# Kernel tuning notes

Measured on AMD Instinct MI355X. Metric: run time of the kernel, lower is better.

## Reference

```python
import jax, jax.numpy as jnp
import numpy as np

K = 3          # kernel size
SH, SW = 2, 1  # stride
PH, PW = 1, 1  # padding


def conv2d(x, w, b, stride, pad):
    y = jax.lax.conv_general_dilated(
        x, w, window_strides=stride,
        padding=[(pad[0], pad[0]), (pad[1], pad[1])],
        dimension_numbers=('NCHW', 'OIHW', 'NCHW'))
    return y + b[None, :, None, None]


def setup_inputs() -> dict:
    key = jax.random.key(0)
    ks = jax.random.split(key, 4)
    x = jax.random.normal(ks[0], (8, 64, 128, 128), jnp.float32)
    # scale offset weights small so sampled offsets are O(1) pixels (exercises
    # the bilinear path without sampling far out of bounds)
    w_offset = jax.random.normal(ks[1], (18, 64, 3, 3), jnp.float32) * 0.02
    b_offset = jnp.zeros((18,), jnp.float32)
    w_mask = jax.random.normal(ks[2], (9, 64, 3, 3), jnp.float32) * 0.05
    b_mask = jnp.zeros((9,), jnp.float32)
    w_conv = jax.random.normal(ks[3], (64, 64, 3, 3), jnp.float32) * (1.0 / 24.0)
    return dict(x=x, w_offset=w_offset, b_offset=b_offset,
                w_mask=w_mask, b_mask=b_mask, w_conv=w_conv)


def _bilinear_gather(x, py, px):
    # x: [B,C,H,W]; py, px: [B,K2,Ho,Wo] float sampling coordinates.
    # Zero-padding outside the image (torchvision deform_conv2d semantics).
    B, C, H, W = x.shape
    y0f = jnp.floor(py)
    x0f = jnp.floor(px)
    dy = py - y0f
    dx = px - x0f
    y0 = y0f.astype(jnp.int32)
    x0 = x0f.astype(jnp.int32)

    def corner(yi, xi, wgt):
        valid = (yi >= 0) & (yi < H) & (xi >= 0) & (xi < W)
        yc = jnp.clip(yi, 0, H - 1)
        xc = jnp.clip(xi, 0, W - 1)
        # per-batch fancy gather -> [B, C, K2, Ho, Wo]
        g = jax.vmap(lambda xb, yb, xbi: xb[:, yb, xbi])(x, yc, xc)
        return g * (wgt * valid)[:, None]

    return (corner(y0,     x0,     (1 - dy) * (1 - dx))
            + corner(y0,     x0 + 1, (1 - dy) * dx)
            + corner(y0 + 1, x0,     dy * (1 - dx))
            + corner(y0 + 1, x0 + 1, dy * dx))


def reference(x, w_offset, b_offset, w_mask, b_mask, w_conv):
    B, C, H, W = x.shape
    offset = conv2d(x, w_offset, b_offset, (SH, SW), (PH, PW))   # [B, 2*K2, Ho, Wo]
    mask = jax.nn.sigmoid(conv2d(x, w_mask, b_mask, (SH, SW), (PH, PW)))  # [B, K2, Ho, Wo]
    Ho, Wo = offset.shape[2], offset.shape[3]
    K2 = K * K
    off = offset.reshape(B, K2, 2, Ho, Wo)
    off_y = off[:, :, 0]   # [B,K2,Ho,Wo]
    off_x = off[:, :, 1]
    ky = (jnp.arange(K2) // K).astype(jnp.float32)
    kx = (jnp.arange(K2) % K).astype(jnp.float32)
    hs = (jnp.arange(Ho) * SH - PH).astype(jnp.float32)
    ws = (jnp.arange(Wo) * SW - PW).astype(jnp.float32)
    py = off_y + ky[None, :, None, None] + hs[None, None, :, None]
    px = off_x + kx[None, :, None, None] + ws[None, None, None, :]
    sampled = _bilinear_gather(x, py, px) * mask[:, None]  # [B,C,K2,Ho,Wo]
    # weighted accumulate over in-channels and kernel taps
    out = jnp.einsum('ock,bckhw->bohw', w_conv.reshape(-1, C, K2), sampled)
    return out
```

## Files before the change

### kernel.cpp

```cpp
#include <hip/hip_runtime.h>
#include <hip/hip_bf16.h>
#include <math.h>

#define BB 8
#define CC 64
#define HH 128
#define WW 128
#define HO 64
#define WO 128
#define OC 64
#define HW (HH * WW)
#define HOWO (HO * WO)

typedef __attribute__((ext_vector_type(8))) short short8;
typedef __attribute__((ext_vector_type(4))) float floatx4;

union BfBits { __hip_bfloat16 h; unsigned short s; };
__device__ __forceinline__ unsigned short f2bf(float f) {
    BfBits b; b.h = __float2bfloat16(f); return b.s;
}
__device__ __forceinline__ float bflo(unsigned int u) {
    return __uint_as_float(u << 16);
}
__device__ __forceinline__ float bfhi(unsigned int u) {
    return __uint_as_float(u & 0xFFFF0000u);
}

__global__ __launch_bounds__(512) void prep(
    const float* __restrict__ x,
    const float* __restrict__ w_off, const float* __restrict__ w_msk,
    const float* __restrict__ w_conv,
    unsigned short* __restrict__ xT, unsigned int* __restrict__ xP,
    unsigned short* __restrict__ Wom, unsigned short* __restrict__ W2)
{
    __shared__ float T[64][129];
    int tid = threadIdx.x;
    int bx = blockIdx.x;
    if (bx < 1024) {
        int b = bx & 7, y = bx >> 3;
        int wl = tid & 127, c0 = tid >> 7;
#pragma unroll
        for (int i = 0; i < 16; ++i) {
            int c = 4 * i + c0;
            T[c][wl] = x[(((size_t)b * CC + c) * HH + y) * WW + wl];
        }
        __syncthreads();
        int c = tid & 63, wg = tid >> 6;
#pragma unroll
        for (int i = 0; i < 16; ++i) {
            int wp = wg * 16 + i;
            unsigned int lo = f2bf(T[c][wp]);
            unsigned int hi = (wp < 127) ? f2bf(T[c][wp + 1]) : 0u;
            size_t e = (((size_t)b * HH + y) * WW + wp) * 64 + c;
            xT[e] = (unsigned short)lo;
            xP[e] = lo | (hi << 16);
        }
    } else if (bx < 1060) {
        int i = (bx - 1024) * 512 + tid;
        int ch = i / 576, kk = i % 576;
        int xs = kk >> 6, c = kk & 63;
        float v = 0.0f;
        if (ch < 18)      v = w_off[(ch * CC + c) * 9 + xs];
        else if (ch < 27) v = w_msk[((ch - 18) * CC + c) * 9 + xs];
        Wom[i] = f2bf(v);
    } else {
        int i = (bx - 1060) * 512 + tid;
        int k = i % 9, c = (i / 9) % CC, o = i / (CC * 9);
        W2[((size_t)k * OC + o) * CC + c] = f2bf(w_conv[i]);
    }
}

__global__ __launch_bounds__(256) void fused(
    const unsigned short* __restrict__ xT, const unsigned int* __restrict__ xP,
    const unsigned short* __restrict__ Wom, const unsigned short* __restrict__ W2,
    const float* __restrict__ b_off, const float* __restrict__ b_msk,
    float* __restrict__ out)
{
    __shared__ __align__(16) char lds[47360];
    unsigned short (*S)[32][64] = (unsigned short(*)[32][64])lds;
    typedef unsigned short XsRow[34][72];
    XsRow* Xs = (XsRow*)lds;
    float (*omr)[33] = (float(*)[33])(lds + 36864);
    uint2*  metaR = (uint2*)(lds + 40432);
    float4* metaC = (float4*)(lds + 42736);

    int tid = threadIdx.x;
    int lane = tid & 63;
    int wv = __builtin_amdgcn_readfirstlane(tid >> 6);
    int bx = blockIdx.x;
    int b = bx & 7;
    int rest = bx >> 3;
    int h = rest >> 2;
    int w0 = (rest & 3) * 32;
    int h2 = 2 * h - 1;
    int m16 = lane & 15, q = lane >> 4;

    for (int u = tid; u < 816; u += 256) {
        int ky = u / 272;
        int rem = u - ky * 272;
        int col = rem >> 3, cb = rem & 7;
        int hy = h2 + ky, wc = w0 - 1 + col;
        short8 v = {0, 0, 0, 0, 0, 0, 0, 0};
        if ((unsigned)hy < (unsigned)HH && (unsigned)wc < (unsigned)WW)
            v = *(const short8*)(xT + (((size_t)b * HH + hy) * WW + wc) * 64 + cb * 8);
        *(short8*)&Xs[ky][col][cb * 8] = v;
    }
    __syncthreads();

    {
        int mt = wv & 1, nt = wv >> 1;
        floatx4 a = (floatx4){0.f, 0.f, 0.f, 0.f};
        const unsigned short* wa = Wom + (mt * 16 + m16) * 576 + q * 8;
#pragma unroll
        for (int t = 0; t < 18; ++t) {
            int xs = t >> 1, ky = xs / 3, kx = xs % 3;
            short8 af = *(const short8*)(wa + t * 32);
            short8 bf = *(const short8*)&Xs[ky][nt * 16 + m16 + kx][(t & 1) * 32 + q * 8];
            a = __builtin_amdgcn_mfma_f32_16x16x32_bf16(af, bf, a, 0, 0, 0);
        }
#pragma unroll
        for (int r = 0; r < 4; ++r) {
            int ch = mt * 16 + q * 4 + r;
            if (ch < 27) omr[ch][nt * 16 + m16] = a[r];
        }
    }
    __syncthreads();

    for (int u = tid; u < 288; u += 256) {
        int kk = u >> 5, pos = u & 31;
        float offy = omr[2 * kk][pos] + b_off[2 * kk];
        float offx = omr[2 * kk + 1][pos] + b_off[2 * kk + 1];
        float mk = 1.0f / (1.0f + __expf(-(omr[18 + kk][pos] + b_msk[kk])));
        float py = offy + (float)(kk / 3) + (float)h2;
        float px = offx + (float)(kk % 3) + (float)(w0 + pos - 1);

        float y0f = floorf(py), x0f = floorf(px);
        float dy = py - y0f, dx = px - x0f;
        int y0 = (int)y0f, x0 = (int)x0f;
        int y1 = y0 + 1, x1 = x0 + 1;
        bool vy0 = (unsigned)y0 < (unsigned)HH;
        bool vy1 = (unsigned)y1 < (unsigned)HH;
        bool vx0 = (unsigned)x0 < (unsigned)WW;
        bool vx1 = (unsigned)x1 < (unsigned)WW;
        float w00 = (1.0f - dy) * (1.0f - dx) * ((vy0 && vx0) ? mk : 0.0f);
        float w01 = (1.0f - dy) * dx          * ((vy0 && vx1) ? mk : 0.0f);
        float w10 = dy * (1.0f - dx)          * ((vy1 && vx0) ? mk : 0.0f);
        float w11 = dy * dx                   * ((vy1 && vx1) ? mk : 0.0f);
        int xbase = min(max(x0, 0), WW - 2);
        bool s0 = x0 > xbase;
        bool s1 = x1 > xbase;
        float4 cf;
        cf.x = (s0 ? 0.f : w00) + (s1 ? 0.f : w01);
        cf.y = (s0 ? w00 : 0.f) + (s1 ? w01 : 0.f);
        cf.z = (s0 ? 0.f : w10) + (s1 ? 0.f : w11);
        cf.w = (s0 ? w10 : 0.f) + (s1 ? w11 : 0.f);
        int yc0 = min(max(y0, 0), HH - 1);
        int yc1 = min(max(y1, 0), HH - 1);
        metaC[u] = cf;
        uint2 mr;
        mr.x = (unsigned)(yc0 * WW + xbase) * 256u;
        mr.y = (unsigned)(yc1 * WW + xbase) * 256u;
        metaR[u] = mr;
    }
    __syncthreads();

    int p0 = wv * 8;
    int c = lane;
    int c4 = 4 * c;
    const char* xPb = (const char*)(xP + (size_t)b * HW * 64);
    unsigned int G0[2][8], G1[2][8];

    auto issue = [&](int k, int sel) {
#pragma unroll
        for (int i = 0; i < 8; ++i) {
            uint2 mr = metaR[k * 32 + p0 + i];
            unsigned r0 = __builtin_amdgcn_readfirstlane(mr.x);
            unsigned r1 = __builtin_amdgcn_readfirstlane(mr.y);
            G0[sel][i] = *(const unsigned int*)(xPb + r0 + c4);
            G1[sel][i] = *(const unsigned int*)(xPb + r1 + c4);
        }
    };
    auto store = [&](int k, int sel) {
#pragma unroll
        for (int i = 0; i < 8; ++i) {
            float4 cf = metaC[k * 32 + p0 + i];
            float v = cf.x * bflo(G0[sel][i]) + cf.y * bfhi(G0[sel][i])
                    + cf.z * bflo(G1[sel][i]) + cf.w * bfhi(G1[sel][i]);
            int pos = p0 + i;
            S[k][pos][((c >> 3) ^ (pos & 7)) * 8 + (c & 7)] = f2bf(v);
        }
    };

    issue(0, 0);
#pragma unroll
    for (int k = 0; k < 9; ++k) {
        if (k < 8) issue(k + 1, (k + 1) & 1);
        store(k, k & 1);
    }
    __syncthreads();

    floatx4 acc0 = (floatx4){0.f, 0.f, 0.f, 0.f};
    floatx4 acc1 = (floatx4){0.f, 0.f, 0.f, 0.f};
#pragma unroll
    for (int k = 0; k < 9; ++k) {
        const unsigned short* wk = W2 + ((size_t)(k * OC) + wv * 16 + m16) * CC + q * 8;
#pragma unroll
        for (int s = 0; s < 2; ++s) {
            short8 af = *(const short8*)(wk + s * 32);
            int cb = ((q + 4 * s) ^ (m16 & 7)) * 8;
            short8 bf0 = *(const short8*)&S[k][m16][cb];
            short8 bf1 = *(const short8*)&S[k][16 + m16][cb];
            acc0 = __builtin_amdgcn_mfma_f32_16x16x32_bf16(af, bf0, acc0, 0, 0, 0);
            acc1 = __builtin_amdgcn_mfma_f32_16x16x32_bf16(af, bf1, acc1, 0, 0, 0);
        }
    }

#pragma unroll
    for (int nt = 0; nt < 2; ++nt) {
        floatx4 av = nt ? acc1 : acc0;
#pragma unroll
        for (int r = 0; r < 4; ++r) {
            int o = wv * 16 + q * 4 + r;
            out[(((size_t)b * OC + o) * HO + h) * WO + w0 + nt * 16 + m16] = av[r];
        }
    }
}

extern "C" void kernel_launch(void* const* d_in, const int* in_sizes, int n_in,
                              void* d_out, int out_size, void* d_ws, size_t ws_size,
                              hipStream_t stream)
{
    const float* x      = (const float*)d_in[0];
    const float* w_off  = (const float*)d_in[1];
    const float* b_off  = (const float*)d_in[2];
    const float* w_msk  = (const float*)d_in[3];
    const float* b_msk  = (const float*)d_in[4];
    const float* w_conv = (const float*)d_in[5];
    float* out = (float*)d_out;

    unsigned short* xT = (unsigned short*)d_ws;
    unsigned int* xP = (unsigned int*)(xT + (size_t)BB * HW * 64);
    unsigned short* Wom = (unsigned short*)(xP + (size_t)BB * HW * 64);
    unsigned short* W2 = Wom + 32 * 576;

    prep<<<dim3(1132), dim3(512), 0, stream>>>(x, w_off, w_msk, w_conv,
                                               xT, xP, Wom, W2);
    fused<<<dim3(2048), dim3(256), 0, stream>>>(xT, xP, Wom, W2,
                                                b_off, b_msk, out);
}
```

Before: 145.5 us.

## Pack 2x2 bilinear quads per pixel and pipeline gather with MFMA in halved LDS

Result: slower. 173.1 us (+18.9%).

```diff
diff --git a/kernel.cpp b/kernel.cpp
--- a/kernel.cpp
+++ b/kernel.cpp
@@ -1,5 +1,6 @@
 #include <hip/hip_runtime.h>
 #include <hip/hip_bf16.h>
+#include <hip/hip_fp16.h>
 #include <math.h>
 
 #define BB 8
@@ -30,30 +31,37 @@
     const float* __restrict__ x,
     const float* __restrict__ w_off, const float* __restrict__ w_msk,
     const float* __restrict__ w_conv,
-    unsigned short* __restrict__ xT, unsigned int* __restrict__ xP,
+    unsigned short* __restrict__ xT, uint2* __restrict__ xQ,
     unsigned short* __restrict__ Wom, unsigned short* __restrict__ W2)
 {
-    __shared__ float T[64][129];
+    __shared__ float T0[64][129];
+    __shared__ float T1[64][129];
     int tid = threadIdx.x;
     int bx = blockIdx.x;
     if (bx < 1024) {
         int b = bx & 7, y = bx >> 3;
         int wl = tid & 127, c0 = tid >> 7;
+        bool has1 = (y < 127);
 #pragma unroll
         for (int i = 0; i < 16; ++i) {
             int c = 4 * i + c0;
-            T[c][wl] = x[(((size_t)b * CC + c) * HH + y) * WW + wl];
+            const float* px = x + (((size_t)b * CC + c) * HH + y) * WW + wl;
+            T0[c][wl] = px[0];
+            T1[c][wl] = has1 ? px[WW] : 0.0f;
         }
         __syncthreads();
         int c = tid & 63, wg = tid >> 6;
 #pragma unroll
         for (int i = 0; i < 16; ++i) {
             int wp = wg * 16 + i;
-            unsigned int lo = f2bf(T[c][wp]);
-            unsigned int hi = (wp < 127) ? f2bf(T[c][wp + 1]) : 0u;
+            unsigned int lo0 = f2bf(T0[c][wp]);
+            unsigned int hi0 = (wp < 127) ? f2bf(T0[c][wp + 1]) : 0u;
+            unsigned int lo1 = f2bf(T1[c][wp]);
+            unsigned int hi1 = (wp < 127) ? f2bf(T1[c][wp + 1]) : 0u;
             size_t e = (((size_t)b * HH + y) * WW + wp) * 64 + c;
-            xT[e] = (unsigned short)lo;
-            xP[e] = lo | (hi << 16);
+            xT[e] = (unsigned short)lo0;
+            uint2 qv; qv.x = lo0 | (hi0 << 16); qv.y = lo1 | (hi1 << 16);
+            xQ[e] = qv;
         }
     } else if (bx < 1060) {
         int i = (bx - 1024) * 512 + tid;
@@ -71,18 +79,18 @@
 }
 
 __global__ __launch_bounds__(256) void fused(
-    const unsigned short* __restrict__ xT, const unsigned int* __restrict__ xP,
+    const unsigned short* __restrict__ xT, const uint2* __restrict__ xQ,
     const unsigned short* __restrict__ Wom, const unsigned short* __restrict__ W2,
     const float* __restrict__ b_off, const float* __restrict__ b_msk,
     float* __restrict__ out)
 {
-    __shared__ __align__(16) char lds[47360];
-    unsigned short (*S)[32][64] = (unsigned short(*)[32][64])lds;
+    __shared__ __align__(16) char lds[18304];
     typedef unsigned short XsRow[34][72];
     XsRow* Xs = (XsRow*)lds;
-    float (*omr)[33] = (float(*)[33])(lds + 36864);
-    uint2*  metaR = (uint2*)(lds + 40432);
-    float4* metaC = (float4*)(lds + 42736);
+    unsigned short (*S)[32][64] = (unsigned short(*)[32][64])lds;
+    unsigned int* metaR = (unsigned int*)(lds + 8192);
+    uint2* metaC = (uint2*)(lds + 9344);
+    float (*omr)[33] = (float(*)[33])(lds + 14720);
 
     int tid = threadIdx.x;
     int lane = tid & 63;
@@ -146,73 +154,82 @@
         float w01 = (1.0f - dy) * dx          * ((vy0 && vx1) ? mk : 0.0f);
         float w10 = dy * (1.0f - dx)          * ((vy1 && vx0) ? mk : 0.0f);
         float w11 = dy * dx                   * ((vy1 && vx1) ? mk : 0.0f);
-        int xbase = min(max(x0, 0), WW - 2);
-        bool s0 = x0 > xbase;
-        bool s1 = x1 > xbase;
-        float4 cf;
-        cf.x = (s0 ? 0.f : w00) + (s1 ? 0.f : w01);
-        cf.y = (s0 ? w00 : 0.f) + (s1 ? w01 : 0.f);
-        cf.z = (s0 ? 0.f : w10) + (s1 ? 0.f : w11);
-        cf.w = (s0 ? w10 : 0.f) + (s1 ? w11 : 0.f);
-        int yc0 = min(max(y0, 0), HH - 1);
-        int yc1 = min(max(y1, 0), HH - 1);
-        metaC[u] = cf;
-        uint2 mr;
-        mr.x = (unsigned)(yc0 * WW + xbase) * 256u;
-        mr.y = (unsigned)(yc1 * WW + xbase) * 256u;
-        metaR[u] = mr;
+        int yb = min(max(y0, 0), HH - 2);
+        int xb = min(max(x0, 0), WW - 2);
+        int a0 = min(max(y0 - yb, 0), 1);
+        int a1 = min(max(y1 - yb, 0), 1);
+        int e0 = min(max(x0 - xb, 0), 1);
+        int e1 = min(max(x1 - xb, 0), 1);
+        float r0A = ((e0 == 0) ? w00 : 0.f) + ((e1 == 0) ? w01 : 0.f);
+        float r0B = ((e0 == 1) ? w00 : 0.f) + ((e1 == 1) ? w01 : 0.f);
+        float r1A = ((e0 == 0) ? w10 : 0.f) + ((e1 == 0) ? w11 : 0.f);
+        float r1B = ((e0 == 1) ? w10 : 0.f) + ((e1 == 1) ? w11 : 0.f);
+        float c00 = ((a0 == 0) ? r0A : 0.f) + ((a1 == 0) ? r1A : 0.f);
+        float c01 = ((a0 == 0) ? r0B : 0.f) + ((a1 == 0) ? r1B : 0.f);
+        float c10 = ((a0 == 1) ? r0A : 0.f) + ((a1 == 1) ? r1A : 0.f);
+        float c11 = ((a0 == 1) ? r0B : 0.f) + ((a1 == 1) ? r1B : 0.f);
+
+        __half2 hA = __floats2half2_rn(c00, c01);
+        __half2 hB = __floats2half2_rn(c10, c11);
+        uint2 cc;
+        cc.x = __builtin_bit_cast(unsigned int, hA);
+        cc.y = __builtin_bit_cast(unsigned int, hB);
+        metaC[u] = cc;
+        metaR[u] = (unsigned)(yb * WW + xb) * 512u;
     }
     __syncthreads();
 
     int p0 = wv * 8;
     int c = lane;
-    int c4 = 4 * c;
-    const char* xPb = (const char*)(xP + (size_t)b * HW * 64);
-    unsigned int G0[2][8], G1[2][8];
-
-    auto issue = [&](int k, int sel) {
-#pragma unroll
-        for (int i = 0; i < 8; ++i) {
-            uint2 mr = metaR[k * 32 + p0 + i];
-            unsigned r0 = __builtin_amdgcn_readfirstlane(mr.x);
-            unsigned r1 = __builtin_amdgcn_readfirstlane(mr.y);
-            G0[sel][i] = *(const unsigned int*)(xPb + r0 + c4);
-            G1[sel][i] = *(const unsigned int*)(xPb + r1 + c4);
-        }
-    };
-    auto store = [&](int k, int sel) {
-#pragma unroll
-        for (int i = 0; i < 8; ++i) {
-            float4 cf = metaC[k * 32 + p0 + i];
-            float v = cf.x * bflo(G0[sel][i]) + cf.y * bfhi(G0[sel][i])
-                    + cf.z * bflo(G1[sel][i]) + cf.w * bfhi(G1[sel][i]);
-            int pos = p0 + i;
-            S[k][pos][((c >> 3) ^ (pos & 7)) * 8 + (c & 7)] = f2bf(v);
-        }
-    };
-
-    issue(0, 0);
-#pragma unroll
-    for (int k = 0; k < 9; ++k) {
-        if (k < 8) issue(k + 1, (k + 1) & 1);
-        store(k, k & 1);
-    }
-    __syncthreads();
-
+    int c8 = 8 * c;
+    const char* xQb = (const char*)(xQ + (size_t)b * HW * 64);
     floatx4 acc0 = (floatx4){0.f, 0.f, 0.f, 0.f};
     floatx4 acc1 = (floatx4){0.f, 0.f, 0.f, 0.f};
+    uint2 G[2][8];
+
+    auto issue = [&](int k, int sel) {
+#pragma unroll
+        for (int i = 0; i < 8; ++i) {
+            unsigned rb = __builtin_amdgcn_readfirstlane(metaR[k * 32 + p0 + i]);
+            G[sel][i] = *(const uint2*)(xQb + rb + c8);
+        }
+    };
+    auto store = [&](int k, int buf, int sel) {
+#pragma unroll
+        for (int i = 0; i < 8; ++i) {
+            uint2 cc = metaC[k * 32 + p0 + i];
+            __half2 hA = __builtin_bit_cast(__half2, cc.x);
+            __half2 hB = __builtin_bit_cast(__half2, cc.y);
+            float v = __low2float(hA) * bflo(G[sel][i].x)
+                    + __high2float(hA) * bfhi(G[sel][i].x)
+                    + __low2float(hB) * bflo(G[sel][i].y)
+                    + __high2float(hB) * bfhi(G[sel][i].y);
+            int pos = p0 + i;
+            S[buf][pos][((c >> 3) ^ (pos & 7)) * 8 + (c & 7)] = f2bf(v);
+        }
+    };
+
+    issue(0, 0);
+    store(0, 0, 0);
+
 #pragma unroll
     for (int k = 0; k < 9; ++k) {
-        const unsigned short* wk = W2 + ((size_t)(k * OC) + wv * 16 + m16) * CC + q * 8;
-#pragma unroll
-        for (int s = 0; s < 2; ++s) {
-            short8 af = *(const short8*)(wk + s * 32);
-            int cb = ((q + 4 * s) ^ (m16 & 7)) * 8;
-            short8 bf0 = *(const short8*)&S[k][m16][cb];
-            short8 bf1 = *(const short8*)&S[k][16 + m16][cb];
-            acc0 = __builtin_amdgcn_mfma_f32_16x16x32_bf16(af, bf0, acc0, 0, 0, 0);
-            acc1 = __builtin_amdgcn_mfma_f32_16x16x32_bf16(af, bf1, acc1, 0, 0, 0);
-        }
+        __syncthreads();
+        if (k < 8) issue(k + 1, (k + 1) & 1);
+        {
+            const unsigned short* wk = W2 + ((size_t)(k * OC) + wv * 16 + m16) * CC + q * 8;
+            int buf = k & 1;
+#pragma unroll
+            for (int s = 0; s < 2; ++s) {
+                short8 af = *(const short8*)(wk + s * 32);
+                int cb = ((q + 4 * s) ^ (m16 & 7)) * 8;
+                short8 bf0 = *(const short8*)&S[buf][m16][cb];
+                short8 bf1 = *(const short8*)&S[buf][16 + m16][cb];
+                acc0 = __builtin_amdgcn_mfma_f32_16x16x32_bf16(af, bf0, acc0, 0, 0, 0);
+                acc1 = __builtin_amdgcn_mfma_f32_16x16x32_bf16(af, bf1, acc1, 0, 0, 0);
+            }
+        }
+        if (k < 8) store(k + 1, (k + 1) & 1, (k + 1) & 1);
     }
 
 #pragma unroll
@@ -238,13 +255,13 @@
     const float* w_conv = (const float*)d_in[5];
     float* out = (float*)d_out;
 
-    unsigned short* xT = (unsigned short*)d_ws;
-    unsigned int* xP = (unsigned int*)(xT + (size_t)BB * HW * 64);
-    unsigned short* Wom = (unsigned short*)(xP + (size_t)BB * HW * 64);
+    uint2* xQ = (uint2*)d_ws;
+    unsigned short* xT = (unsigned short*)(xQ + (size_t)BB * HW * 64);
+    unsigned short* Wom = xT + (size_t)BB * HW * 64;
     unsigned short* W2 = Wom + 32 * 576;
 
     prep<<<dim3(1132), dim3(512), 0, stream>>>(x, w_off, w_msk, w_conv,
-                                               xT, xP, Wom, W2);
-    fused<<<dim3(2048), dim3(256), 0, stream>>>(xT, xP, Wom, W2,
+                                               xT, xQ, Wom, W2);
+    fused<<<dim3(2048), dim3(256), 0, stream>>>(xT, xQ, Wom, W2,
                                                 b_off, b_msk, out);
 }
```
